# Kernel tuning notes

Measured on AMD Instinct MI355X. Metric: run time of the kernel, lower is better.

The kernel has to match this reference:

```python
import jax, jax.numpy as jnp
import numpy as np


def setup_inputs() -> dict:
    key = jax.random.key(0)
    ks = jax.random.split(key, 5)
    B, S, F = 32, 2048, 64
    s = lambda d: 1.0 / np.sqrt(d)
    return {
        "x": jax.random.normal(ks[0], (B, S, F), jnp.float32),
        "Wq": jax.random.normal(ks[1], (F, 24), jnp.float32) * s(F),
        "Wk": jax.random.normal(ks[2], (F, 24), jnp.float32) * s(F),
        "Wv": jax.random.normal(ks[3], (F, 32), jnp.float32) * s(F),
        "Wh": jax.random.normal(ks[4], (32, F), jnp.float32) * s(32),
    }


def reference(x, Wq, Wk, Wv, Wh):
    # x: [B, S, F]
    q = jnp.einsum("bsf,fd->bsd", x, Wq)  # [B, S, 24]
    k = jnp.einsum("bsf,fd->bsd", x, Wk)  # [B, S, 24]
    v = jnp.einsum("bsf,fd->bsd", x, Wv)  # [B, S, 32]
    a = jnp.einsum("bqd,bkd->bqk", q, k)  # [B, S, S]
    # NOTE: softmax over dim=1 (query axis), as in the original module
    a = jax.nn.softmax(a, axis=1)
    h1 = jnp.einsum("bqk,bkd->bqd", a, v)  # [B, S, 32]
    return jnp.einsum("bsd,df->bsf", h1, Wh)  # [B, S, F]
```

## Files before the change

### kernel.cpp

```cpp
#include <hip/hip_runtime.h>
#include <hip/hip_fp16.h>

#define SS 2048
#define L2E 1.44269504088896340736f

typedef _Float16 f16x4 __attribute__((ext_vector_type(4)));
typedef _Float16 f16x8 __attribute__((ext_vector_type(8)));
typedef float f32x4 __attribute__((ext_vector_type(4)));

#define GLDS16(g, l) __builtin_amdgcn_global_load_lds(                          \
    (const __attribute__((address_space(1))) void*)(g),                         \
    (__attribute__((address_space(3))) void*)(l), 16, 0, 0)
#define GLDS4(g, l) __builtin_amdgcn_global_load_lds(                           \
    (const __attribute__((address_space(1))) void*)(g),                         \
    (__attribute__((address_space(3))) void*)(l), 4, 0, 0)

__global__ __launch_bounds__(256) void qkv_kernel(
    const float* __restrict__ x, const float* __restrict__ Wq,
    const float* __restrict__ Wk, const float* __restrict__ Wv,
    _Float16* __restrict__ qfp, _Float16* __restrict__ kfp,
    _Float16* __restrict__ vfp)
{
    __shared__ float wcs[64 * 96];
    __shared__ __align__(16) _Float16 wfb[12 * 512];

    int t = threadIdx.x;
    int wv = t >> 6, l = t & 63, llo = l & 15, lhi = l >> 4;

    for (int i = t; i < 384; i += 256) {
        float4 v = ((const float4*)Wq)[i];
        int f = (i * 4) / 24, c = (i * 4) % 24;
        *(float4*)&wcs[f * 96 + c] = v;
    }
    for (int i = t; i < 384; i += 256) {
        float4 v = ((const float4*)Wk)[i];
        int f = (i * 4) / 24, c = (i * 4) % 24;
        *(float4*)&wcs[f * 96 + 32 + c] = v;
    }
    for (int i = t; i < 512; i += 256) {
        float4 v = ((const float4*)Wv)[i];
        int f = i >> 3, c = (i * 4) & 31;
        *(float4*)&wcs[f * 96 + 64 + c] = v;
    }
    {
        int f = t >> 2, which = t & 3;
        int c = (which < 2) ? (24 + which * 4) : (56 + (which - 2) * 4);
        *(float4*)&wcs[f * 96 + c] = (float4){0.f, 0.f, 0.f, 0.f};
    }
    __syncthreads();

    #pragma unroll
    for (int p = 0; p < 3; ++p) {
        int sidx = t + p * 256;
        int fr = sidx >> 6, lane = sidx & 63;
        int ct = fr >> 1, kk = fr & 1;
        int lls = lane & 15, lhs = lane >> 4;
        f16x8 wfr;
        #pragma unroll
        for (int j = 0; j < 8; ++j)
            wfr[j] = (_Float16)wcs[(kk * 32 + lhs * 8 + j) * 96 + ct * 16 + lls];
        *(f16x8*)&wfb[fr * 512 + lane * 8] = wfr;
    }
    __syncthreads();

    _Float16* os = (_Float16*)wcs;

    if (t < 128) {
        int reg = t >> 6, rr = t & 63;
        *(f16x8*)&os[reg * 2048 + (rr >> 4) * 512 + (48 + (rr & 15)) * 8]
            = (f16x8){0, 0, 0, 0, 0, 0, 0, 0};
    }

    long rowbase = (long)blockIdx.x * 64;
    const float* xr = x + (rowbase + wv * 16 + llo) * 64 + lhi * 8;
    f16x8 a0, a1;
    {
        float4 u0 = *(const float4*)(xr);
        float4 u1 = *(const float4*)(xr + 4);
        float4 u2 = *(const float4*)(xr + 32);
        float4 u3 = *(const float4*)(xr + 36);
        a0[0] = (_Float16)u0.x; a0[1] = (_Float16)u0.y;
        a0[2] = (_Float16)u0.z; a0[3] = (_Float16)u0.w;
        a0[4] = (_Float16)u1.x; a0[5] = (_Float16)u1.y;
        a0[6] = (_Float16)u1.z; a0[7] = (_Float16)u1.w;
        a1[0] = (_Float16)u2.x; a1[1] = (_Float16)u2.y;
        a1[2] = (_Float16)u2.z; a1[3] = (_Float16)u2.w;
        a1[4] = (_Float16)u3.x; a1[5] = (_Float16)u3.y;
        a1[6] = (_Float16)u3.z; a1[7] = (_Float16)u3.w;
    }

    f32x4 d[6];
    #pragma unroll
    for (int ct = 0; ct < 6; ++ct) {
        f16x8 b0 = *(const f16x8*)&wfb[(ct * 2 + 0) * 512 + l * 8];
        f16x8 b1 = *(const f16x8*)&wfb[(ct * 2 + 1) * 512 + l * 8];
        d[ct] = __builtin_amdgcn_mfma_f32_16x16x32_f16(a0, b0,
                  (f32x4){0.f, 0.f, 0.f, 0.f}, 0, 0, 0);
        d[ct] = __builtin_amdgcn_mfma_f32_16x16x32_f16(a1, b1, d[ct], 0, 0, 0);
    }

    #pragma unroll
    for (int r = 0; r < 4; ++r) {
        int sl = lhi * 4 + r;
        os[wv * 512 + ((llo >> 3) * 16 + sl) * 8 + (llo & 7)]
            = (_Float16)(d[0][r] * L2E);
        if (llo < 8)
            os[wv * 512 + (32 + sl) * 8 + llo] = (_Float16)(d[1][r] * L2E);
        os[2048 + wv * 512 + ((llo >> 3) * 16 + sl) * 8 + (llo & 7)]
            = (_Float16)d[2][r];
        if (llo < 8)
            os[2048 + wv * 512 + (32 + sl) * 8 + llo] = (_Float16)d[3][r];
        os[4096 + wv * 512 + (lhi * 16 + llo) * 8 + r]     = (_Float16)d[4][r];
        os[4096 + wv * 512 + (lhi * 16 + llo) * 8 + 4 + r] = (_Float16)d[5][r];
    }
    __syncthreads();

    long blk = blockIdx.x;
    *(f16x8*)(qfp + blk * 2048 + t * 8) = *(const f16x8*)&os[t * 8];
    *(f16x8*)(kfp + blk * 2048 + t * 8) = *(const f16x8*)&os[2048 + t * 8];
    *(f16x8*)(vfp + blk * 2048 + t * 8) = *(const f16x8*)&os[4096 + t * 8];
}

__global__ __launch_bounds__(256) void stats_kernel(
    const _Float16* __restrict__ qf, const _Float16* __restrict__ kf,
    float* __restrict__ zpart)
{
    int w = blockIdx.x;
    int b = w & 31, kb = (w >> 5) & 7, qs = w >> 8;
    int t = threadIdx.x;
    int wv = t >> 6, l = t & 63, llo = l & 15, lhi = l >> 4;

    const _Float16* kfb = kf + ((long)b * 128 + kb * 16 + wv * 4) * 512 + l * 8;
    f16x8 af[4];
    #pragma unroll
    for (int kt = 0; kt < 4; ++kt) af[kt] = *(const f16x8*)(kfb + kt * 512);

    const _Float16* qb = qf + ((long)b * 128 + qs * 32) * 512 + l * 8;
    f32x4 z[4] = {{0,0,0,0},{0,0,0,0},{0,0,0,0},{0,0,0,0}};

    #pragma unroll 4
    for (int qi = 0; qi < 32; ++qi) {
        f16x8 q0 = *(const f16x8*)(qb + qi * 512);
        #pragma unroll
        for (int kt = 0; kt < 4; ++kt) {
            f32x4 d = __builtin_amdgcn_mfma_f32_16x16x32_f16(af[kt], q0,
                        (f32x4){0.f, 0.f, 0.f, 0.f}, 0, 0, 0);
            #pragma unroll
            for (int r = 0; r < 4; ++r) z[kt][r] += __builtin_amdgcn_exp2f(d[r]);
        }
    }
    #pragma unroll
    for (int m = 1; m < 16; m <<= 1)
        #pragma unroll
        for (int kt = 0; kt < 4; ++kt)
            #pragma unroll
            for (int r = 0; r < 4; ++r) z[kt][r] += __shfl_xor(z[kt][r], m, 64);
    if (llo == 0) {
        #pragma unroll
        for (int kt = 0; kt < 4; ++kt)
            *(f32x4*)(zpart + ((long)qs * 32 + b) * SS + kb * 256 + wv * 64
                      + kt * 16 + lhi * 4) = z[kt];
    }
}

__global__ __launch_bounds__(256) void finalize_kernel(
    const float* __restrict__ zpart, float* __restrict__ wneg)
{
    int i = blockIdx.x * 256 + threadIdx.x;
    float s = 0.f;
    #pragma unroll
    for (int qs = 0; qs < 4; ++qs) s += zpart[(long)qs * 32 * SS + i];
    wneg[i] = -__builtin_amdgcn_logf(s);
}

__global__ __launch_bounds__(256) void attn_out_kernel(
    const _Float16* __restrict__ qf, const _Float16* __restrict__ kf,
    const _Float16* __restrict__ vf, const float* __restrict__ wneg,
    const float* __restrict__ Wh, float* __restrict__ out)
{
    __shared__ __align__(16) _Float16 lds[2][8448];

    int w = blockIdx.x;
    int b = w >> 5, qblk = w & 31;
    int t = threadIdx.x;
    int wv = t >> 6, l = t & 63, llo = l & 15, lhi = l >> 4;
    int q0 = qblk * 64 + wv * 16;

    f16x8 qfr = *(const f16x8*)(qf + ((long)b * 128 + qblk * 4 + wv) * 512 + l * 8);

    f16x4 whlo[4], whhi[4];
    #pragma unroll
    for (int fb = 0; fb < 4; ++fb)
        #pragma unroll
        for (int j = 0; j < 4; ++j) {
            whlo[fb][j] = (_Float16)Wh[(4 * lhi + j) * 64 + fb * 16 + llo];
            whhi[fb][j] = (_Float16)Wh[(16 + 4 * lhi + j) * 64 + fb * 16 + llo];
        }

    const _Float16* kgb = kf + ((long)b * 128 + wv) * 512 + l * 8;
    const _Float16* vgb = vf + (long)b * 65536 + wv * 512 + l * 8;
    const float*    wgb = wneg + (long)b * SS + l;

    f32x4 acc0 = {0,0,0,0}, acc1 = {0,0,0,0};

    GLDS16(kgb,        &lds[0][wv * 512]);
    GLDS16(kgb + 2048, &lds[0][2048 + wv * 512]);
    GLDS16(vgb,        &lds[0][4096 + wv * 512]);
    GLDS16(vgb + 2048, &lds[0][6144 + wv * 512]);
    if (wv == 0) {
        GLDS4(wgb,      (float*)&lds[0][8192]);
        GLDS4(wgb + 64, (float*)&lds[0][8320]);
    }

    for (int ph = 0; ph < 16; ++ph) {
        int cb = ph & 1;
        __syncthreads();
        if (ph < 15) {
            long base = (long)(ph + 1) * 4096;
            GLDS16(kgb + base,        &lds[cb ^ 1][wv * 512]);
            GLDS16(kgb + base + 2048, &lds[cb ^ 1][2048 + wv * 512]);
            GLDS16(vgb + base,        &lds[cb ^ 1][4096 + wv * 512]);
            GLDS16(vgb + base + 2048, &lds[cb ^ 1][6144 + wv * 512]);
            if (wv == 0) {
                GLDS4(wgb + (ph + 1) * 128,      (float*)&lds[cb ^ 1][8192]);
                GLDS4(wgb + (ph + 1) * 128 + 64, (float*)&lds[cb ^ 1][8320]);
            }
        }
        const _Float16* Kb = &lds[cb][0];
        const _Float16* Vb = &lds[cb][4096];
        const float*    Wb = (const float*)&lds[cb][8192];
        #pragma unroll
        for (int t4 = 0; t4 < 8; ++t4) {
            f16x8 kfr = *(const f16x8*)(Kb + t4 * 512 + l * 8);
            float4 w4 = *(const float4*)(Wb + t4 * 16 + lhi * 4);
            f32x4 d = __builtin_amdgcn_mfma_f32_16x16x32_f16(kfr, qfr,
                        (f32x4){w4.x, w4.y, w4.z, w4.w}, 0, 0, 0);
            f16x4 pa;
            #pragma unroll
            for (int r = 0; r < 4; ++r) pa[r] = (_Float16)__builtin_amdgcn_exp2f(d[r]);
            f16x8 v01 = *(const f16x8*)(Vb + t4 * 512 + l * 8);
            f16x4 v0 = {v01[0], v01[1], v01[2], v01[3]};
            f16x4 v1 = {v01[4], v01[5], v01[6], v01[7]};
            acc0 = __builtin_amdgcn_mfma_f32_16x16x16f16(v0, pa, acc0, 0, 0, 0);
            acc1 = __builtin_amdgcn_mfma_f32_16x16x16f16(v1, pa, acc1, 0, 0, 0);
        }
    }

    f16x4 h0, h1;
    #pragma unroll
    for (int r = 0; r < 4; ++r) {
        h0[r] = (_Float16)acc0[r];
        h1[r] = (_Float16)acc1[r];
    }
    float* orow = out + ((long)b * SS + q0 + llo) * 64 + 4 * lhi;
    #pragma unroll
    for (int fb = 0; fb < 4; ++fb) {
        f32x4 o = __builtin_amdgcn_mfma_f32_16x16x16f16(whlo[fb], h0,
                    (f32x4){0.f, 0.f, 0.f, 0.f}, 0, 0, 0);
        o = __builtin_amdgcn_mfma_f32_16x16x16f16(whhi[fb], h1, o, 0, 0, 0);
        *(f32x4*)(orow + fb * 16) = o;
    }
}

extern "C" void kernel_launch(void* const* d_in, const int* in_sizes, int n_in,
                              void* d_out, int out_size, void* d_ws, size_t ws_size,
                              hipStream_t stream) {
    const float* x  = (const float*)d_in[0];
    const float* Wq = (const float*)d_in[1];
    const float* Wk = (const float*)d_in[2];
    const float* Wv = (const float*)d_in[3];
    const float* Wh = (const float*)d_in[4];
    float* out = (float*)d_out;

    char* ws = (char*)d_ws;
    _Float16* qf  = (_Float16*)(ws);
    _Float16* kf  = (_Float16*)(ws + (4l << 20));
    _Float16* vf  = (_Float16*)(ws + (8l << 20));
    float* wneg   = (float*)(ws + (12l << 20));
    float* zpart  = (float*)(ws + (12l << 20) + (256l << 10));

    qkv_kernel<<<1024, 256, 0, stream>>>(x, Wq, Wk, Wv, qf, kf, vf);
    stats_kernel<<<1024, 256, 0, stream>>>(qf, kf, zpart);
    finalize_kernel<<<256, 256, 0, stream>>>(zpart, wneg);
    attn_out_kernel<<<1024, 256, 0, stream>>>(qf, kf, vf, wneg, Wh, out);
}
```

Baseline: 71.37 us.

## Fuse softmax-stat finalize into stats kernel with full-query LDS-staged loop

The stats kernel now has each block cover 64 keys over all 2048 queries, where before it split the query axis into four partial sums. The exp-sum is reduced in-kernel and written straight out as negative log, which removes the zpart buffer and the separate finalize launch. Query tiles are staged through double-buffered LDS with global_load_lds, so the block's waves share them instead of each wave reading from global. Each wave now holds one key fragment instead of four, so there is less register reuse per query load, and every tile iteration adds a barrier.

```diff
diff --git a/kernel.cpp b/kernel.cpp
--- a/kernel.cpp
+++ b/kernel.cpp
@@ -123,54 +123,46 @@
 
 __global__ __launch_bounds__(256) void stats_kernel(
     const _Float16* __restrict__ qf, const _Float16* __restrict__ kf,
-    float* __restrict__ zpart)
+    float* __restrict__ wneg)
 {
+    __shared__ __align__(16) _Float16 qtile[2][2048];
     int w = blockIdx.x;
-    int b = w & 31, kb = (w >> 5) & 7, qs = w >> 8;
+    int b = w >> 5, kb = w & 31;
     int t = threadIdx.x;
     int wv = t >> 6, l = t & 63, llo = l & 15, lhi = l >> 4;
 
-    const _Float16* kfb = kf + ((long)b * 128 + kb * 16 + wv * 4) * 512 + l * 8;
-    f16x8 af[4];
-    #pragma unroll
-    for (int kt = 0; kt < 4; ++kt) af[kt] = *(const f16x8*)(kfb + kt * 512);
-
-    const _Float16* qb = qf + ((long)b * 128 + qs * 32) * 512 + l * 8;
-    f32x4 z[4] = {{0,0,0,0},{0,0,0,0},{0,0,0,0},{0,0,0,0}};
-
-    #pragma unroll 4
-    for (int qi = 0; qi < 32; ++qi) {
-        f16x8 q0 = *(const f16x8*)(qb + qi * 512);
-        #pragma unroll
-        for (int kt = 0; kt < 4; ++kt) {
-            f32x4 d = __builtin_amdgcn_mfma_f32_16x16x32_f16(af[kt], q0,
+    f16x8 af = *(const f16x8*)(kf + ((long)b * 128 + kb * 4 + wv) * 512 + l * 8);
+    const _Float16* qsrc = qf + (long)b * 65536 + wv * 512 + l * 8;
+
+    f32x4 z = {0.f, 0.f, 0.f, 0.f};
+
+    GLDS16(qsrc, &qtile[0][wv * 512]);
+    for (int tile = 0; tile < 32; ++tile) {
+        int cb = tile & 1;
+        asm volatile("s_waitcnt vmcnt(0)" ::: "memory");
+        __syncthreads();
+        __builtin_amdgcn_sched_barrier(0);
+        if (tile < 31)
+            GLDS16(qsrc + (long)(tile + 1) * 2048, &qtile[cb ^ 1][wv * 512]);
+        #pragma unroll
+        for (int fi = 0; fi < 4; ++fi) {
+            f16x8 q0 = *(const f16x8*)&qtile[cb][fi * 512 + l * 8];
+            f32x4 d = __builtin_amdgcn_mfma_f32_16x16x32_f16(af, q0,
                         (f32x4){0.f, 0.f, 0.f, 0.f}, 0, 0, 0);
             #pragma unroll
-            for (int r = 0; r < 4; ++r) z[kt][r] += __builtin_amdgcn_exp2f(d[r]);
+            for (int r = 0; r < 4; ++r) z[r] += __builtin_amdgcn_exp2f(d[r]);
         }
     }
     #pragma unroll
     for (int m = 1; m < 16; m <<= 1)
         #pragma unroll
-        for (int kt = 0; kt < 4; ++kt)
-            #pragma unroll
-            for (int r = 0; r < 4; ++r) z[kt][r] += __shfl_xor(z[kt][r], m, 64);
+        for (int r = 0; r < 4; ++r) z[r] += __shfl_xor(z[r], m, 64);
     if (llo == 0) {
         #pragma unroll
-        for (int kt = 0; kt < 4; ++kt)
-            *(f32x4*)(zpart + ((long)qs * 32 + b) * SS + kb * 256 + wv * 64
-                      + kt * 16 + lhi * 4) = z[kt];
-    }
-}
-
-__global__ __launch_bounds__(256) void finalize_kernel(
-    const float* __restrict__ zpart, float* __restrict__ wneg)
-{
-    int i = blockIdx.x * 256 + threadIdx.x;
-    float s = 0.f;
-    #pragma unroll
-    for (int qs = 0; qs < 4; ++qs) s += zpart[(long)qs * 32 * SS + i];
-    wneg[i] = -__builtin_amdgcn_logf(s);
+        for (int r = 0; r < 4; ++r)
+            wneg[(long)b * SS + (kb * 4 + wv) * 16 + lhi * 4 + r]
+                = -__builtin_amdgcn_logf(z[r]);
+    }
 }
 
 __global__ __launch_bounds__(256) void attn_out_kernel(
@@ -277,10 +269,8 @@
     _Float16* kf  = (_Float16*)(ws + (4l << 20));
     _Float16* vf  = (_Float16*)(ws + (8l << 20));
     float* wneg   = (float*)(ws + (12l << 20));
-    float* zpart  = (float*)(ws + (12l << 20) + (256l << 10));
 
     qkv_kernel<<<1024, 256, 0, stream>>>(x, Wq, Wk, Wv, qf, kf, vf);
-    stats_kernel<<<1024, 256, 0, stream>>>(qf, kf, zpart);
-    finalize_kernel<<<256, 256, 0, stream>>>(zpart, wneg);
+    stats_kernel<<<1024, 256, 0, stream>>>(qf, kf, wneg);
     attn_out_kernel<<<1024, 256, 0, stream>>>(qf, kf, vf, wneg, Wh, out);
 }
```

Measured after the change: 70.00 us. Within noise of the previous version (-1.9%).
